# Kernel tuning notes

Measured on AMD Instinct MI355X. Metric: run time of the kernel, lower is better.

## Reference

```python
import jax, jax.numpy as jnp
import numpy as np

CUTOFF = 10.0
LOG2 = float(np.log(2.0))

N_NODES = 50000
N_EDGES = 800000
IN_CH = 128
FILTERS = 128
OUT_CH = 128
N_GAUSS = 50


def _xavier(key, shape):
    fan_in, fan_out = shape[1], shape[0]
    bound = float(np.sqrt(6.0 / (fan_in + fan_out)))
    return jax.random.uniform(key, shape, jnp.float32, -bound, bound)


def setup_inputs() -> dict:
    key = jax.random.key(0)
    ks = jax.random.split(key, 10)
    h = jax.random.normal(ks[0], (N_NODES, IN_CH), jnp.float32)
    edge_index = jax.random.randint(ks[1], (2, N_EDGES), 0, N_NODES, jnp.int32)
    edge_weight = jax.random.uniform(ks[2], (N_EDGES,), jnp.float32) * CUTOFF
    edge_attr = jax.random.normal(ks[3], (N_EDGES, N_GAUSS), jnp.float32)
    return {
        "h": h,
        "edge_index": edge_index,
        "edge_weight": edge_weight,
        "edge_attr": edge_attr,
        "lin1_w": _xavier(ks[4], (FILTERS, IN_CH)),
        "nn_w1": _xavier(ks[5], (FILTERS, N_GAUSS)),
        "nn_b1": jnp.zeros((FILTERS,), jnp.float32),
        "nn_w2": _xavier(ks[6], (FILTERS, FILTERS)),
        "nn_b2": jnp.zeros((FILTERS,), jnp.float32),
        "lin2_w": _xavier(ks[7], (OUT_CH, FILTERS)),
        "lin2_b": jnp.zeros((OUT_CH,), jnp.float32),
    }


def reference(h, edge_index, edge_weight, edge_attr,
              lin1_w, nn_w1, nn_b1, nn_w2, nn_b2, lin2_w, lin2_b):
    n_nodes = h.shape[0]
    # lin1 (no bias): [N, filters]
    h1 = h @ lin1_w.T
    # cosine cutoff per edge: [E]
    c = 0.5 * (jnp.cos(edge_weight * jnp.pi / CUTOFF) + 1.0)
    # filter-generating MLP with shifted softplus: [E, filters]
    x = jax.nn.softplus(edge_attr @ nn_w1.T + nn_b1) - LOG2
    W = (jax.nn.softplus(x @ nn_w2.T + nn_b2) - LOG2) * c[:, None]
    # gather source node feats, weight, scatter-add to destination
    msg = W * h1[edge_index[1]]                                  # [E, filters]
    agg = jax.ops.segment_sum(msg, edge_index[0], num_segments=n_nodes)
    h2 = h1 + agg
    return h2 @ lin2_w.T + lin2_b
```

## Files before the change

### kernel.cpp

```cpp
#include <hip/hip_runtime.h>

#define NNODES 50000
#define NEDGES 800000
#define NG 50
#define PI_OVER_CUT 0.31415926535897931f
#define LN2 0.69314718055994531f

static_assert(NEDGES % 16 == 0, "edge tiling assumes E % 16 == 0");
static_assert((NG & 1) == 0, "pair loads assume NG even");
#define NTILES (NEDGES / 16)
static_assert(NTILES % 8 == 0, "XCD partition assumes NTILES % 8 == 0");
#define SCAN_N 50176
#define SCAN_BLK 196

typedef float f32x4 __attribute__((ext_vector_type(4)));
typedef float f32x2 __attribute__((ext_vector_type(2)));
typedef float f32x4u __attribute__((ext_vector_type(4), aligned(4)));
typedef short s16x8 __attribute__((ext_vector_type(8)));

static __device__ __forceinline__ unsigned cvt_pk(float lo, float hi) {
  unsigned r;
  asm("v_cvt_pk_bf16_f32 %0, %1, %2" : "=v"(r) : "v"(lo), "v"(hi));
  return r;
}

static __device__ __forceinline__ short f2bf(float f) {
  union { float f; unsigned u; } v; v.f = f;
  return (short)((v.u + 0x7fffu + ((v.u >> 16) & 1u)) >> 16);
}

static __device__ __forceinline__ float bf2f(unsigned short u) {
  union { unsigned u; float f; } v; v.u = (unsigned)u << 16;
  return v.f;
}

static __device__ __forceinline__ float sp_shift(float x) {
  return fmaxf(x, 0.f) + __logf(1.f + __expf(-fabsf(x))) - LN2;
}

static __device__ __forceinline__ float sp_w(float x) {
  return __log2f(1.f + __expf(x));
}

#define MFMA16(A, B, C) __builtin_amdgcn_mfma_f32_16x16x32_bf16((A), (B), (C), 0, 0, 0)


__global__ __launch_bounds__(256) void lin1_mfma(const float* __restrict__ X,
                                                 const float* __restrict__ W,
                                                 unsigned short* __restrict__ Y2,
                                                 float* __restrict__ aggz) {
  __shared__ __align__(16) short sB[16384];
  const int tid = threadIdx.x;
  if (aggz) {
    const size_t b0 = (size_t)blockIdx.x * 64 * 128;
    const size_t lim = (size_t)NNODES * 128;
    for (int i = tid; i < 64 * 32; i += 256) {
      size_t off = b0 + (size_t)i * 4;
      if (off < lim) *(f32x4*)(aggz + off) = f32x4{0.f, 0.f, 0.f, 0.f};
    }
  }
  for (int i = tid; i < 8192; i += 256) {
    int p = i & 3, l = (i >> 2) & 63, t = (i >> 8) & 7, s = i >> 11;
    int k = s * 32 + (l >> 4) * 8 + p * 2;
    int f = t * 16 + (l & 15);
    f32x2 v = *(const f32x2*)(W + f * 128 + k);
    ((unsigned*)sB)[i] = cvt_pk(v.x, v.y);
  }
  __syncthreads();
  const int lane = tid & 63, wave = tid >> 6, lrow = lane & 15, lk = lane >> 4;
  const s16x8* B = (const s16x8*)sB;
  const int rowA = blockIdx.x * 64 + wave * 16 + lrow;
  s16x8 a[4];
#pragma unroll
  for (int s = 0; s < 4; ++s) {
    unsigned* ap = (unsigned*)&a[s];
    f32x4 v0 = {}, v1 = {};
    if (rowA < NNODES) {
      const float* xr = X + (size_t)rowA * 128 + s * 32 + lk * 8;
      v0 = *(const f32x4*)xr;
      v1 = *(const f32x4*)(xr + 4);
    }
    ap[0] = cvt_pk(v0.x, v0.y); ap[1] = cvt_pk(v0.z, v0.w);
    ap[2] = cvt_pk(v1.x, v1.y); ap[3] = cvt_pk(v1.z, v1.w);
  }
  f32x4 acc[8] = {};
#pragma unroll
  for (int s = 0; s < 4; ++s)
#pragma unroll
    for (int t = 0; t < 8; ++t)
      acc[t] = MFMA16(a[s], B[(s * 8 + t) * 64 + lane], acc[t]);
  const int rowD = blockIdx.x * 64 + wave * 16 + lk * 4;
#pragma unroll
  for (int r = 0; r < 4; ++r) {
    int node = rowD + r;
    if (node < NNODES) {
      uint4 q;
      q.x = cvt_pk(acc[0][r], acc[1][r]);
      q.y = cvt_pk(acc[2][r], acc[3][r]);
      q.z = cvt_pk(acc[4][r], acc[5][r]);
      q.w = cvt_pk(acc[6][r], acc[7][r]);
      *(uint4*)(Y2 + (size_t)node * 128 + lrow * 8) = q;
    }
  }
}

__global__ __launch_bounds__(256) void lin2_mfma(const unsigned short* __restrict__ H1bT,
                                                 const float* AG,
                                                 const float* __restrict__ W,
                                                 const float* __restrict__ Bias,
                                                 float* OUT) {
  __shared__ __align__(16) short sB[16384];
  const int tid = threadIdx.x;
  for (int i = tid; i < 8192; i += 256) {
    int p = i & 3, l = (i >> 2) & 63, t = (i >> 8) & 7, s = i >> 11;
    int k = s * 32 + (l >> 4) * 8 + p * 2;
    int f = t * 16 + (l & 15);
    f32x2 v = *(const f32x2*)(W + f * 128 + k);
    ((unsigned*)sB)[i] = cvt_pk(v.x, v.y);
  }
  __syncthreads();
  const int lane = tid & 63, wave = tid >> 6, lrow = lane & 15, lk = lane >> 4;
  const s16x8* B = (const s16x8*)sB;
  const int rowA = blockIdx.x * 64 + wave * 16 + lrow;
  s16x8 a[4];
#pragma unroll
  for (int s = 0; s < 4; ++s) {
    unsigned* ap = (unsigned*)&a[s];
    float w[8] = {};
    if (rowA < NNODES) {
      const float* gr = AG + (size_t)rowA * 128 + s * 32 + lk * 8;
      f32x4 g0 = *(const f32x4*)gr;
      f32x4 g1 = *(const f32x4*)(gr + 4);
#pragma unroll
      for (int j = 0; j < 8; ++j) {
        int c = s * 32 + lk * 8 + j;
        float hv = bf2f(H1bT[(size_t)rowA * 128 + (c & 15) * 8 + (c >> 4)]);
        w[j] = hv + (j < 4 ? g0[j] : g1[j - 4]);
      }
    }
    ap[0] = cvt_pk(w[0], w[1]); ap[1] = cvt_pk(w[2], w[3]);
    ap[2] = cvt_pk(w[4], w[5]); ap[3] = cvt_pk(w[6], w[7]);
  }
  f32x4 acc[8] = {};
#pragma unroll
  for (int s = 0; s < 4; ++s)
#pragma unroll
    for (int t = 0; t < 8; ++t)
      acc[t] = MFMA16(a[s], B[(s * 8 + t) * 64 + lane], acc[t]);
  const int rowD = blockIdx.x * 64 + wave * 16 + lk * 4;
#pragma unroll
  for (int t = 0; t < 8; ++t) {
    float bb = Bias[t * 16 + lrow];
#pragma unroll
    for (int r = 0; r < 4; ++r)
      if (rowD + r < NNODES)
        OUT[(size_t)(rowD + r) * 128 + t * 16 + lrow] = acc[t][r] + bb;
  }
}

__global__ void k_hist(const int* __restrict__ ei, int* __restrict__ cnt) {
  int e = blockIdx.x * 256 + threadIdx.x;
  if (e < NEDGES) atomicAdd(&cnt[ei[e]], 1);
}

__global__ __launch_bounds__(256) void k_scanA(int* __restrict__ cnt,
                                               int* __restrict__ bsum) {
  __shared__ int sh[256];
  const int t = threadIdx.x;
  const int i = blockIdx.x * 256 + t;
  int v = cnt[i];
  sh[t] = v;
  __syncthreads();
  for (int off = 1; off < 256; off <<= 1) {
    int u = (t >= off) ? sh[t - off] : 0;
    __syncthreads();
    sh[t] += u;
    __syncthreads();
  }
  cnt[i] = sh[t] - v;
  if (t == 255) bsum[blockIdx.x] = sh[255];
}

__global__ __launch_bounds__(256) void k_scanB(int* __restrict__ bsum) {
  __shared__ int sh[256];
  const int t = threadIdx.x;
  int v = (t < SCAN_BLK) ? bsum[t] : 0;
  sh[t] = v;
  __syncthreads();
  for (int off = 1; off < 256; off <<= 1) {
    int u = (t >= off) ? sh[t - off] : 0;
    __syncthreads();
    sh[t] += u;
    __syncthreads();
  }
  if (t < SCAN_BLK) bsum[t] = sh[t] - v;
}

__global__ __launch_bounds__(256) void k_scanC(int* __restrict__ cnt,
                                               const int* __restrict__ bsum) {
  int i = blockIdx.x * 256 + threadIdx.x;
  cnt[i] += bsum[blockIdx.x];
}

__global__ void k_prepM(const int* __restrict__ ei, const float* __restrict__ ew,
                        int* __restrict__ cursor, int4* __restrict__ meta) {
  int e = blockIdx.x * 256 + threadIdx.x;
  if (e >= NEDGES) return;
  int d = ei[e], s = ei[NEDGES + e];
  float c = 0.5f * (__cosf(ew[e] * PI_OVER_CUT) + 1.f);
  int pos = atomicAdd(&cursor[d], 1);
  meta[pos] = make_int4(d, s, __float_as_int(c), e);
}

#define LOADSET_M(S, TL)                                                       \
  {                                                                            \
    const int base_ = (TL) * 16;                                               \
    const int4* mp_ = meta + base_ + lk * 4;                                   \
    int4 m0_ = mp_[0], m1_ = mp_[1], m2_ = mp_[2], m3_ = mp_[3];               \
    dst_##S[0] = m0_.x; dst_##S[1] = m1_.x; dst_##S[2] = m2_.x; dst_##S[3] = m3_.x; \
    src_##S[0] = m0_.y; src_##S[1] = m1_.y; src_##S[2] = m2_.y; src_##S[3] = m3_.y; \
    cw_##S[0] = __int_as_float(m0_.z); cw_##S[1] = __int_as_float(m1_.z);      \
    cw_##S[2] = __int_as_float(m2_.z); cw_##S[3] = __int_as_float(m3_.z);      \
    const int ser_ = meta[base_ + lrow].w;                                     \
    const float* ar_ = attr + (size_t)ser_ * NG;                               \
    unsigned* a0_ = (unsigned*)&av0_##S;                                       \
    unsigned* a1_ = (unsigned*)&av1_##S;                                       \
    if (ser_ < NEDGES - 1) {           \
      f32x4u p0 = *(const f32x4u*)(ar_ + lk * 8);                              \
      f32x4u p1 = *(const f32x4u*)(ar_ + lk * 8 + 4);                          \
      f32x4u p2 = *(const f32x4u*)(ar_ + 32 + lk * 8);                         \
      f32x4u p3 = *(const f32x4u*)(ar_ + 32 + lk * 8 + 4);                     \
      a0_[0] = cvt_pk(p0.x, p0.y); a0_[1] = cvt_pk(p0.z, p0.w);                \
      a0_[2] = cvt_pk(p1.x, p1.y); a0_[3] = cvt_pk(p1.z, p1.w);                \
      a1_[0] = cvt_pk(p2.x, p2.y); a1_[1] = cvt_pk(p2.z, p2.w);                \
      a1_[2] = cvt_pk(p3.x, p3.y); a1_[3] = cvt_pk(p3.z, p3.w);                \
    } else {                                                                   \
      _Pragma("unroll") for (int jj = 0; jj < 4; ++jj) {                       \
        f32x2 v = *(const f32x2*)(ar_ + lk * 8 + jj * 2);                      \
        a0_[jj] = cvt_pk(v.x, v.y);                                            \
      }                                                                        \
      _Pragma("unroll") for (int jj = 0; jj < 4; ++jj) {                       \
        int k_ = 32 + lk * 8 + jj * 2;                                         \
        f32x2 v = {0.f, 0.f};                                                  \
        if (k_ < NG) v = *(const f32x2*)(ar_ + k_);                            \
        a1_[jj] = cvt_pk(v.x, v.y);                                            \
      }                                                                        \
    }                                                                          \
  }

#define COMPUTESET_M(S)                                                        \
  {                                                                            \
    s16x8 hv8[4];                                                              \
    _Pragma("unroll") for (int r = 0; r < 4; ++r)                              \
      hv8[r] = *(const s16x8*)(h1bT + (size_t)src_##S[r] * 128 + lrow * 8);    \
    f32x4 acc[8] = {};                                                         \
    _Pragma("unroll") for (int t = 0; t < 8; ++t)                              \
      acc[t] = MFMA16(av0_##S, B1r[t], acc[t]);                                \
    _Pragma("unroll") for (int t = 0; t < 8; ++t)                              \
      acc[t] = MFMA16(av1_##S, B1r[8 + t], acc[t]);                            \
    _Pragma("unroll") for (int t = 0; t < 8; ++t) {                            \
      int f = t * 16 + lrow;                                                   \
      float bb = sb1[f];                                                       \
      float w0 = sp_w(acc[t][0] + bb);                                         \
      float w1 = sp_w(acc[t][1] + bb);                                         \
      float w2 = sp_w(acc[t][2] + bb);                                         \
      float w3 = sp_w(acc[t][3] + bb);                                         \
      float v0 = __builtin_fmaf(w0, LN2, -LN2);                                \
      float v1 = __builtin_fmaf(w1, LN2, -LN2);                                \
      float v2 = __builtin_fmaf(w2, LN2, -LN2);                                \
      float v3 = __builtin_fmaf(w3, LN2, -LN2);                                \
      unsigned p01 = cvt_pk(v0, v1), p23 = cvt_pk(v2, v3);                     \
      const int row0_ = lk * 4;                                                \
      int a0 = ((row0_ + 0) * 256 + f * 2) ^ (((row0_ + 0) & 7) << 4);         \
      int a1 = ((row0_ + 1) * 256 + f * 2) ^ (((row0_ + 1) & 7) << 4);         \
      int a2 = ((row0_ + 2) * 256 + f * 2) ^ (((row0_ + 2) & 7) << 4);         \
      int a3 = ((row0_ + 3) * 256 + f * 2) ^ (((row0_ + 3) & 7) << 4);         \
      *(short*)(sXw + a0) = (short)p01;                                        \
      *(short*)(sXw + a1) = (short)(p01 >> 16);                                \
      *(short*)(sXw + a2) = (short)p23;                                        \
      *(short*)(sXw + a3) = (short)(p23 >> 16);                                \
    }                                                                          \
    f32x4 acc2[8] = {};                                                        \
    _Pragma("unroll") for (int s = 0; s < 4; ++s) {                            \
      int ab = (lrow * 256 + s * 64 + lk * 16) ^ ((lrow & 7) << 4);            \
      s16x8 av = *(const s16x8*)(sXw + ab);                                    \
      _Pragma("unroll") for (int t = 0; t < 8; ++t)                            \
        acc2[t] = MFMA16(av, B2[(s * 8 + t) * 64 + lane], acc2[t]);            \
    }                                                                          \
    const float lc0 = cw_##S[0] * LN2, lc1 = cw_##S[1] * LN2;                  \
    const float lc2 = cw_##S[2] * LN2, lc3 = cw_##S[3] * LN2;                  \
    const int d0 = dst_##S[0], d3 = dst_##S[3];                                \
    const bool b1f = dst_##S[1] != d0, b2f = dst_##S[2] != dst_##S[1],         \
               b3f = d3 != dst_##S[2];                                         \
    const bool allsame = !(b1f | b2f | b3f);                                   \
    const int next_head = __shfl(d0, (lane + 16) & 63);                        \
    const bool tor = (lk < 3) && (next_head == d3);                            \
    const int td0 = __shfl(d3, lrow);                                          \
    const int td1 = __shfl(d3, lrow + 16);                                     \
    const int td2 = __shfl(d3, lrow + 32);                                     \
    const bool m0 = (lk >= 1) && (td0 == d0);                                  \
    const bool m1 = (lk >= 2) && (td1 == d0);                                  \
    const bool m2 = (lk >= 3) && (td2 == d0);                                  \
    const bool emit_head = !(allsame && tor);                                  \
    const bool emit_tail = (!allsame) && !tor;                                 \
    const bool mid1 = b1f && b2f, mid2 = b2f && b3f,                           \
               mid12 = b1f && (!b2f) && b3f;                                   \
    _Pragma("unroll") for (int t = 0; t < 8; ++t) {                            \
      int f = t * 16 + lrow;                                                   \
      float bb = sb2[f];                                                       \
      float w0 = sp_w(acc2[t][0] + bb);                                        \
      float w1 = sp_w(acc2[t][1] + bb);                                        \
      float w2 = sp_w(acc2[t][2] + bb);                                        \
      float w3 = sp_w(acc2[t][3] + bb);                                        \
      float v0 = __builtin_fmaf(w0, lc0, -lc0) * bf2f((unsigned short)hv8[0][t]); \
      float v1 = __builtin_fmaf(w1, lc1, -lc1) * bf2f((unsigned short)hv8[1][t]); \
      float v2 = __builtin_fmaf(w2, lc2, -lc2) * bf2f((unsigned short)hv8[2][t]); \
      float v3 = __builtin_fmaf(w3, lc3, -lc3) * bf2f((unsigned short)hv8[3][t]); \
      float head_sum = v0 + (b1f ? 0.f : v1 + (b2f ? 0.f : v2 + (b3f ? 0.f : v3))); \
      float tail_sum = v3 + (b3f ? 0.f : v2 + (b2f ? 0.f : v1 + (b1f ? 0.f : v0))); \
      float ts0 = __shfl(tail_sum, lrow);                                      \
      float ts1 = __shfl(tail_sum, lrow + 16);                                 \
      float ts2 = __shfl(tail_sum, lrow + 32);                                 \
      float carry = (m0 ? ts0 : 0.f) + (m1 ? ts1 : 0.f) + (m2 ? ts2 : 0.f);    \
      if (emit_head) atomicAdd(&agg[(size_t)d0 * 128 + f], head_sum + carry);  \
      if (emit_tail) atomicAdd(&agg[(size_t)d3 * 128 + f], tail_sum);          \
      if (mid1) atomicAdd(&agg[(size_t)dst_##S[1] * 128 + f], v1);             \
      if (mid2) atomicAdd(&agg[(size_t)dst_##S[2] * 128 + f], v2);             \
      if (mid12) atomicAdd(&agg[(size_t)dst_##S[1] * 128 + f], v1 + v2);       \
    }                                                                          \
  }

__global__ __launch_bounds__(256, 2) void cfconv_edge_m(
    const int4* __restrict__ meta, const float* __restrict__ attr,
    const float* __restrict__ w1, const float* __restrict__ b1,
    const float* __restrict__ w2, const float* __restrict__ b2,
    const unsigned short* __restrict__ h1bT, float* __restrict__ agg) {
  __shared__ __align__(16) short sB2[16384];
  __shared__ __align__(16) short sX[4][2048];
  __shared__ float sb1[128], sb2[128];
  const int tid = threadIdx.x;
  if (tid < 128) { sb1[tid] = b1[tid]; sb2[tid] = b2[tid]; }
  for (int i = tid; i < 8192; i += 256) {
    int p = i & 3, l = (i >> 2) & 63, t = (i >> 8) & 7, s = i >> 11;
    int k = s * 32 + (l >> 4) * 8 + p * 2;
    int f = t * 16 + (l & 15);
    f32x2 v = *(const f32x2*)(w2 + f * 128 + k);
    ((unsigned*)sB2)[i] = cvt_pk(v.x, v.y);
  }
  __syncthreads();
  const int lane = tid & 63;
  const int wave = tid >> 6;
  const int lrow = lane & 15;
  const int lk = lane >> 4;
  s16x8 B1r[16];
  {
    unsigned* bp = (unsigned*)B1r;
#pragma unroll
    for (int s = 0; s < 2; ++s)
#pragma unroll
      for (int t = 0; t < 8; ++t) {
        const float* wrow = w1 + (t * 16 + lrow) * NG;
#pragma unroll
        for (int p = 0; p < 4; ++p) {
          int k = s * 32 + lk * 8 + p * 2;
          f32x2 v = {0.f, 0.f};
          if (k < NG) v = *(const f32x2*)(wrow + k);
          bp[(s * 8 + t) * 4 + p] = cvt_pk(v.x, v.y);
        }
      }
  }
  const s16x8* B2 = (const s16x8*)sB2;
  char* sXw = (char*)sX[wave];

  const int xcd  = blockIdx.x & 7;
  const int lb   = blockIdx.x >> 3;
  const int tpx  = NTILES / 8;
  const int tend = (xcd + 1) * tpx;
  const int lstride = (gridDim.x >> 3) * 4;
  const int gw0 = xcd * tpx + lb * 4 + wave;

  s16x8 av0_A, av1_A, av0_B, av1_B;
  int dst_A[4], src_A[4], dst_B[4], src_B[4];
  float cw_A[4], cw_B[4];

  int tl = gw0;
  if (tl < tend) LOADSET_M(A, tl);
  while (tl < tend) {
    int n1 = tl + lstride;
    if (n1 < tend) LOADSET_M(B, n1);
    COMPUTESET_M(A);
    tl = n1;
    if (tl >= tend) break;
    int n2 = tl + lstride;
    if (n2 < tend) LOADSET_M(A, n2);
    COMPUTESET_M(B);
    tl = n2;
  }
}

__global__ __launch_bounds__(256, 2) void cfconv_edge_atomic(
    const int* __restrict__ ei, const float* __restrict__ ew,
    const float* __restrict__ attr,
    const float* __restrict__ w1, const float* __restrict__ b1,
    const float* __restrict__ w2, const float* __restrict__ b2,
    const unsigned short* __restrict__ h1bT, float* __restrict__ agg) {
  __shared__ __align__(16) short sB2[16384];
  __shared__ __align__(16) short sX[4][2048];
  __shared__ float sb1[128], sb2[128];
  const int tid = threadIdx.x;
  if (tid < 128) { sb1[tid] = b1[tid]; sb2[tid] = b2[tid]; }
  for (int i = tid; i < 8192; i += 256) {
    int p = i & 3, l = (i >> 2) & 63, t = (i >> 8) & 7, s = i >> 11;
    int k = s * 32 + (l >> 4) * 8 + p * 2;
    int f = t * 16 + (l & 15);
    f32x2 v = *(const f32x2*)(w2 + f * 128 + k);
    ((unsigned*)sB2)[i] = cvt_pk(v.x, v.y);
  }
  __syncthreads();
  const int lane = tid & 63, wave = tid >> 6, lrow = lane & 15, lk = lane >> 4;
  s16x8 B1r[16];
  {
    unsigned* bp = (unsigned*)B1r;
#pragma unroll
    for (int s = 0; s < 2; ++s)
#pragma unroll
      for (int t = 0; t < 8; ++t) {
        const float* wrow = w1 + (t * 16 + lrow) * NG;
#pragma unroll
        for (int p = 0; p < 4; ++p) {
          int k = s * 32 + lk * 8 + p * 2;
          f32x2 v = {0.f, 0.f};
          if (k < NG) v = *(const f32x2*)(wrow + k);
          bp[(s * 8 + t) * 4 + p] = cvt_pk(v.x, v.y);
        }
      }
  }
  const s16x8* B2 = (const s16x8*)sB2;
  char* sXw = (char*)sX[wave];
  const int gw0 = blockIdx.x * 4 + wave;
  const int gstride = gridDim.x * 4;
  for (int wt = gw0; wt < NTILES; wt += gstride) {
    const int e0 = wt * 16;
    int dst[4], src[4];
    float cw[4];
#pragma unroll
    for (int r = 0; r < 4; ++r) {
      int e = e0 + lk * 4 + r;
      dst[r] = ei[e];
      src[r] = ei[NEDGES + e];
      cw[r] = 0.5f * (__cosf(ew[e] * PI_OVER_CUT) + 1.f);
    }
    s16x8 hv8[4];
#pragma unroll
    for (int r = 0; r < 4; ++r)
      hv8[r] = *(const s16x8*)(h1bT + (size_t)src[r] * 128 + lrow * 8);
    const float* ar = attr + (size_t)(e0 + lrow) * NG;
    s16x8 av0, av1;
    unsigned* a0 = (unsigned*)&av0;
    unsigned* a1 = (unsigned*)&av1;
#pragma unroll
    for (int jj = 0; jj < 4; ++jj) {
      f32x2 v = *(const f32x2*)(ar + lk * 8 + jj * 2);
      a0[jj] = cvt_pk(v.x, v.y);
    }
#pragma unroll
    for (int jj = 0; jj < 4; ++jj) {
      int k = 32 + lk * 8 + jj * 2;
      f32x2 v = {0.f, 0.f};
      if (k < NG) v = *(const f32x2*)(ar + k);
      a1[jj] = cvt_pk(v.x, v.y);
    }
    f32x4 acc[8] = {};
#pragma unroll
    for (int t = 0; t < 8; ++t) acc[t] = MFMA16(av0, B1r[t], acc[t]);
#pragma unroll
    for (int t = 0; t < 8; ++t) acc[t] = MFMA16(av1, B1r[8 + t], acc[t]);
#pragma unroll
    for (int t = 0; t < 8; ++t) {
      int f = t * 16 + lrow;
      float bb = sb1[f];
#pragma unroll
      for (int r = 0; r < 4; ++r) {
        int row = lk * 4 + r;
        float v = sp_shift(acc[t][r] + bb);
        int a = (row * 256 + f * 2) ^ ((row & 7) << 4);
        *(short*)(sXw + a) = f2bf(v);
      }
    }
    f32x4 acc2[8] = {};
#pragma unroll
    for (int s = 0; s < 4; ++s) {
      int ab = (lrow * 256 + s * 64 + lk * 16) ^ ((lrow & 7) << 4);
      s16x8 av = *(const s16x8*)(sXw + ab);
#pragma unroll
      for (int t = 0; t < 8; ++t)
        acc2[t] = MFMA16(av, B2[(s * 8 + t) * 64 + lane], acc2[t]);
    }
#pragma unroll
    for (int t = 0; t < 8; ++t) {
      int f = t * 16 + lrow;
      float bb = sb2[f];
#pragma unroll
      for (int r = 0; r < 4; ++r) {
        float Wv = sp_shift(acc2[t][r] + bb) * cw[r];
        atomicAdd(&agg[(size_t)dst[r] * 128 + f], Wv * bf2f((unsigned short)hv8[r][t]));
      }
    }
  }
}

extern "C" void kernel_launch(void* const* d_in, const int* in_sizes, int n_in,
                              void* d_out, int out_size, void* d_ws, size_t ws_size,
                              hipStream_t stream) {
  const float* h      = (const float*)d_in[0];
  const int*   ei     = (const int*)d_in[1];
  const float* ew     = (const float*)d_in[2];
  const float* attr   = (const float*)d_in[3];
  const float* lin1_w = (const float*)d_in[4];
  const float* nn_w1  = (const float*)d_in[5];
  const float* nn_b1  = (const float*)d_in[6];
  const float* nn_w2  = (const float*)d_in[7];
  const float* nn_b2  = (const float*)d_in[8];
  const float* lin2_w = (const float*)d_in[9];
  const float* lin2_b = (const float*)d_in[10];
  float* out = (float*)d_out;

  const int rbM = (NNODES + 63) / 64;
  const int EB  = (NEDGES + 255) / 256;

  const size_t off_bs   = (size_t)SCAN_N * 4;
  const size_t off_meta = off_bs + 1024;
  const size_t off_h1b  = off_meta + (size_t)NEDGES * 16;
  const size_t need_main = off_h1b + (size_t)NNODES * 256;
  const size_t need_fb   = (size_t)NNODES * 256;

  if (ws_size >= need_main) {
    int*  cnt  = (int*)d_ws;
    int*  bsum = (int*)((char*)d_ws + off_bs);
    int4* meta = (int4*)((char*)d_ws + off_meta);
    unsigned short* h1bT = (unsigned short*)((char*)d_ws + off_h1b);

    hipMemsetAsync(cnt, 0, (size_t)SCAN_N * 4, stream);
    k_hist<<<EB, 256, 0, stream>>>(ei, cnt);
    k_scanA<<<SCAN_BLK, 256, 0, stream>>>(cnt, bsum);
    k_scanB<<<1, 256, 0, stream>>>(bsum);
    k_scanC<<<SCAN_BLK, 256, 0, stream>>>(cnt, bsum);
    k_prepM<<<EB, 256, 0, stream>>>(ei, ew, cnt, meta);
    lin1_mfma<<<rbM, 256, 0, stream>>>(h, lin1_w, h1bT, out);
    cfconv_edge_m<<<512, 256, 0, stream>>>(meta, attr, nn_w1, nn_b1,
                                           nn_w2, nn_b2, h1bT, out);
    lin2_mfma<<<rbM, 256, 0, stream>>>(h1bT, out, lin2_w, lin2_b, out);
  } else if (ws_size >= need_fb) {
    unsigned short* h1bT = (unsigned short*)d_ws;
    lin1_mfma<<<rbM, 256, 0, stream>>>(h, lin1_w, h1bT, out);
    cfconv_edge_atomic<<<512, 256, 0, stream>>>(ei, ew, attr, nn_w1, nn_b1,
                                                nn_w2, nn_b2, h1bT, out);
    lin2_mfma<<<rbM, 256, 0, stream>>>(h1bT, out, lin2_w, lin2_b, out);
  }
}
```

Before: 300.6 us.

## Deepen edge-tile prefetch to three stages and hoist h1 gathers into loads

The sorted-edge kernel's software pipeline goes from double to triple buffering, so two tiles of metadata and edge attributes are in flight while one is computed. The gather of source-node h1 rows moves from the compute step into the load step, which hides its latency behind earlier compute. This raises register pressure (three sets of attribute and h1 fragments) under launch bounds of 2 blocks per SM, which could cause spills or lower occupancy.

```diff
diff --git a/kernel.cpp b/kernel.cpp
--- a/kernel.cpp
+++ b/kernel.cpp
@@ -218,9 +218,12 @@
     const int4* mp_ = meta + base_ + lk * 4;                                   \
     int4 m0_ = mp_[0], m1_ = mp_[1], m2_ = mp_[2], m3_ = mp_[3];               \
     dst_##S[0] = m0_.x; dst_##S[1] = m1_.x; dst_##S[2] = m2_.x; dst_##S[3] = m3_.x; \
-    src_##S[0] = m0_.y; src_##S[1] = m1_.y; src_##S[2] = m2_.y; src_##S[3] = m3_.y; \
     cw_##S[0] = __int_as_float(m0_.z); cw_##S[1] = __int_as_float(m1_.z);      \
     cw_##S[2] = __int_as_float(m2_.z); cw_##S[3] = __int_as_float(m3_.z);      \
+    hv8_##S[0] = *(const s16x8*)(h1bT + (size_t)m0_.y * 128 + lrow * 8);       \
+    hv8_##S[1] = *(const s16x8*)(h1bT + (size_t)m1_.y * 128 + lrow * 8);       \
+    hv8_##S[2] = *(const s16x8*)(h1bT + (size_t)m2_.y * 128 + lrow * 8);       \
+    hv8_##S[3] = *(const s16x8*)(h1bT + (size_t)m3_.y * 128 + lrow * 8);       \
     const int ser_ = meta[base_ + lrow].w;                                     \
     const float* ar_ = attr + (size_t)ser_ * NG;                               \
     unsigned* a0_ = (unsigned*)&av0_##S;                                       \
@@ -250,9 +253,6 @@
 
 #define COMPUTESET_M(S)                                                        \
   {                                                                            \
-    s16x8 hv8[4];                                                              \
-    _Pragma("unroll") for (int r = 0; r < 4; ++r)                              \
-      hv8[r] = *(const s16x8*)(h1bT + (size_t)src_##S[r] * 128 + lrow * 8);    \
     f32x4 acc[8] = {};                                                         \
     _Pragma("unroll") for (int t = 0; t < 8; ++t)                              \
       acc[t] = MFMA16(av0_##S, B1r[t], acc[t]);                                \
@@ -312,10 +312,10 @@
       float w1 = sp_w(acc2[t][1] + bb);                                        \
       float w2 = sp_w(acc2[t][2] + bb);                                        \
       float w3 = sp_w(acc2[t][3] + bb);                                        \
-      float v0 = __builtin_fmaf(w0, lc0, -lc0) * bf2f((unsigned short)hv8[0][t]); \
-      float v1 = __builtin_fmaf(w1, lc1, -lc1) * bf2f((unsigned short)hv8[1][t]); \
-      float v2 = __builtin_fmaf(w2, lc2, -lc2) * bf2f((unsigned short)hv8[2][t]); \
-      float v3 = __builtin_fmaf(w3, lc3, -lc3) * bf2f((unsigned short)hv8[3][t]); \
+      float v0 = __builtin_fmaf(w0, lc0, -lc0) * bf2f((unsigned short)hv8_##S[0][t]); \
+      float v1 = __builtin_fmaf(w1, lc1, -lc1) * bf2f((unsigned short)hv8_##S[1][t]); \
+      float v2 = __builtin_fmaf(w2, lc2, -lc2) * bf2f((unsigned short)hv8_##S[2][t]); \
+      float v3 = __builtin_fmaf(w3, lc3, -lc3) * bf2f((unsigned short)hv8_##S[3][t]); \
       float head_sum = v0 + (b1f ? 0.f : v1 + (b2f ? 0.f : v2 + (b3f ? 0.f : v3))); \
       float tail_sum = v3 + (b3f ? 0.f : v2 + (b2f ? 0.f : v1 + (b1f ? 0.f : v0))); \
       float ts0 = __shfl(tail_sum, lrow);                                      \
@@ -376,25 +376,29 @@
   const int lb   = blockIdx.x >> 3;
   const int tpx  = NTILES / 8;
   const int tend = (xcd + 1) * tpx;
-  const int lstride = (gridDim.x >> 3) * 4;
-  const int gw0 = xcd * tpx + lb * 4 + wave;
-
-  s16x8 av0_A, av1_A, av0_B, av1_B;
-  int dst_A[4], src_A[4], dst_B[4], src_B[4];
-  float cw_A[4], cw_B[4];
+  const int ls   = (gridDim.x >> 3) * 4;
+  const int gw0  = xcd * tpx + lb * 4 + wave;
+
+  s16x8 av0_A, av1_A, av0_B, av1_B, av0_C, av1_C;
+  s16x8 hv8_A[4], hv8_B[4], hv8_C[4];
+  int dst_A[4], dst_B[4], dst_C[4];
+  float cw_A[4], cw_B[4], cw_C[4];
 
   int tl = gw0;
   if (tl < tend) LOADSET_M(A, tl);
+  if (tl + ls < tend) LOADSET_M(B, tl + ls);
   while (tl < tend) {
-    int n1 = tl + lstride;
-    if (n1 < tend) LOADSET_M(B, n1);
+    { int n = tl + 2 * ls; if (n < tend) LOADSET_M(C, n); }
     COMPUTESET_M(A);
-    tl = n1;
+    tl += ls;
     if (tl >= tend) break;
-    int n2 = tl + lstride;
-    if (n2 < tend) LOADSET_M(A, n2);
+    { int n = tl + 2 * ls; if (n < tend) LOADSET_M(A, n); }
     COMPUTESET_M(B);
-    tl = n2;
+    tl += ls;
+    if (tl >= tend) break;
+    { int n = tl + 2 * ls; if (n < tend) LOADSET_M(B, n); }
+    COMPUTESET_M(C);
+    tl += ls;
   }
 }
 
```

After: 420.3 us. 39.8% more time.
